# Optimization experiments

Hardware: AMD Instinct MI355X
Metric: run time of the kernel (lower is better)

## Reference

```python
import jax, jax.numpy as jnp
import numpy as np

TOP_K = 8
NORM_TOPK_PROB = False


def setup_inputs() -> dict:
    key = jax.random.key(0)
    k1, k2 = jax.random.split(key)
    hidden_states = jax.random.normal(k1, (4, 8192, 2048), dtype=jnp.float32)
    # gate weight: [n_experts=64, hidden_dim=2048], like nn.Linear weight
    weight = jax.random.normal(k2, (64, 2048), dtype=jnp.float32) * 0.02
    return {"hidden_states": hidden_states, "weight": weight}


def reference(hidden_states, weight):
    hidden_dim = weight.shape[1]
    x = hidden_states.reshape(-1, hidden_dim)            # [N, D]
    router_logits = jnp.einsum('nd,ed->ne', x, weight)   # [N, E] F.linear
    # softmax in float32 (dtype=torch.float), returned as the "logits"
    router_probs = jax.nn.softmax(router_logits.astype(jnp.float32), axis=-1)
    router_top_value, router_indices = jax.lax.top_k(router_probs, TOP_K)
    if NORM_TOPK_PROB:
        router_top_value = router_top_value / jnp.sum(router_top_value, axis=-1, keepdims=True)
    router_top_value = router_top_value.astype(router_probs.dtype)
    return (router_probs, router_top_value, router_indices)
```

## Files before the change

kernel.cpp:

```cpp
#include <hip/hip_runtime.h>
#include <math.h>


constexpr int HD = 2048, NE = 64, RPB = 64, BK = 64, NT = HD / BK, TOPK = 8;
constexpr float XSC = 4096.f;
constexpr float WSC = 8192.f;
constexpr float DESCALE = 1.0f / (XSC * WSC);

typedef _Float16 f16x8 __attribute__((ext_vector_type(8)));
typedef float f32x4 __attribute__((ext_vector_type(4)));
typedef void __attribute__((address_space(1)))* gas_t;
typedef void __attribute__((address_space(3)))* las_t;

__device__ __forceinline__ void gload_lds16(const float* g, void* l) {
  __builtin_amdgcn_global_load_lds((gas_t)(uintptr_t)g, (las_t)l, 16, 0, 0);
}

__global__ __launch_bounds__(256, 2)
void router_k(const float* __restrict__ X, const float* __restrict__ W,
              float* __restrict__ probs, float* __restrict__ topv,
              float* __restrict__ topi) {
  __shared__ float4 smem4[4096];
  char* smem = (char*)smem4;

  const int tid = threadIdx.x, wv = tid >> 6, lane = tid & 63;
  const int m_l = lane & 15, q_l = lane >> 4;
  const int rowbase = blockIdx.x * RPB;

  const int kq_st = m_l ^ ((4 * wv + q_l) & 15);
  const float* gx = X + (size_t)(rowbase + 4 * wv + q_l) * HD + kq_st * 4;

  const int we = tid >> 2, wq = tid & 3;
  const float* gw = W + (size_t)we * HD + wq * 16;
  const int g0 = we * 8 + ((2 * wq) ^ (we & 7));
  const int g1 = we * 8 + ((2 * wq + 1) ^ (we & 7));

#pragma unroll
  for (int m = 0; m < 4; ++m)
    gload_lds16(gx + (size_t)m * 16 * HD, smem + (4 * m + wv) * 1024);
  float4 wr[4];
#pragma unroll
  for (int j = 0; j < 4; ++j) wr[j] = *(const float4*)(gw + j * 4);

  f32x4 acc_hh[4], acc_cr[4];
#pragma unroll
  for (int nt = 0; nt < 4; ++nt) {
    acc_hh[nt] = {0.f, 0.f, 0.f, 0.f};
    acc_cr[nt] = {0.f, 0.f, 0.f, 0.f};
  }

  for (int t = 0; t < NT; ++t) {
    const int cur = t & 1;
    char* xcur = smem + cur * 16384;
    char* wcur = smem + 32768 + cur * 16384;

    {
      float v[16];
#pragma unroll
      for (int j = 0; j < 4; ++j) {
        v[4 * j] = wr[j].x; v[4 * j + 1] = wr[j].y;
        v[4 * j + 2] = wr[j].z; v[4 * j + 3] = wr[j].w;
      }
      f16x8 h0, h1, l0, l1;
#pragma unroll
      for (int j = 0; j < 8; ++j) {
        float a = v[j] * WSC;     _Float16 ha = (_Float16)a;
        h0[j] = ha; l0[j] = (_Float16)(a - (float)ha);
        float b = v[j + 8] * WSC; _Float16 hb = (_Float16)b;
        h1[j] = hb; l1[j] = (_Float16)(b - (float)hb);
      }
      *(f16x8*)(wcur + g0 * 16) = h0;
      *(f16x8*)(wcur + g1 * 16) = h1;
      *(f16x8*)(wcur + 8192 + g0 * 16) = l0;
      *(f16x8*)(wcur + 8192 + g1 * 16) = l1;
    }
    if (t + 1 < NT) {
#pragma unroll
      for (int j = 0; j < 4; ++j)
        wr[j] = *(const float4*)(gw + (t + 1) * BK + j * 4);
    }
    __syncthreads();
    if (t + 1 < NT) {
      char* xnxt = smem + (1 - cur) * 16384;
#pragma unroll
      for (int m = 0; m < 4; ++m)
        gload_lds16(gx + (size_t)m * 16 * HD + (t + 1) * BK, xnxt + (4 * m + wv) * 1024);
    }

#pragma unroll
    for (int s = 0; s < 2; ++s) {
      const int row_l = 16 * wv + m_l;
      const int kq0 = 8 * s + 2 * q_l;
      const int G0 = row_l * 16 + (kq0 ^ m_l);
      const int G1 = row_l * 16 + ((kq0 + 1) ^ m_l);
      f32x4 xa = *(const f32x4*)(xcur + G0 * 16);
      f32x4 xb = *(const f32x4*)(xcur + G1 * 16);
      f16x8 ah, al;
#pragma unroll
      for (int j = 0; j < 4; ++j) {
        float a = xa[j] * XSC; _Float16 ha = (_Float16)a;
        ah[j] = ha; al[j] = (_Float16)(a - (float)ha);
        float b = xb[j] * XSC; _Float16 hb = (_Float16)b;
        ah[j + 4] = hb; al[j + 4] = (_Float16)(b - (float)hb);
      }
      const int kgB = 4 * s + q_l;
#pragma unroll
      for (int nt = 0; nt < 4; ++nt) {
        const int ee = nt * 16 + m_l;
        const int gb = ee * 8 + (kgB ^ (ee & 7));
        f16x8 bh = *(const f16x8*)(wcur + gb * 16);
        f16x8 bl = *(const f16x8*)(wcur + 8192 + gb * 16);
        acc_hh[nt] = __builtin_amdgcn_mfma_f32_16x16x32_f16(ah, bh, acc_hh[nt], 0, 0, 0);
        acc_cr[nt] = __builtin_amdgcn_mfma_f32_16x16x32_f16(ah, bl, acc_cr[nt], 0, 0, 0);
        acc_cr[nt] = __builtin_amdgcn_mfma_f32_16x16x32_f16(al, bh, acc_cr[nt], 0, 0, 0);
      }
    }
  }

  __syncthreads();
  float* plds = (float*)smem;
#pragma unroll
  for (int nt = 0; nt < 4; ++nt)
#pragma unroll
    for (int r = 0; r < 4; ++r)
      plds[(16 * wv + 4 * q_l + r) * 68 + nt * 16 + m_l] =
          (acc_hh[nt][r] + acc_cr[nt][r]) * DESCALE;
  __syncthreads();

  for (int rr = 0; rr < 16; ++rr) {
    const int row_l = wv * 16 + rr;
    const float lg = plds[row_l * 68 + lane];

    float mx = lg;
#pragma unroll
    for (int off = 32; off; off >>= 1)
      mx = fmaxf(mx, __shfl_xor(mx, off, 64));

    const float ex = expf(lg - mx);
    float sm = ex;
#pragma unroll
    for (int off = 32; off; off >>= 1)
      sm += __shfl_xor(sm, off, 64);

    const float p = ex * (1.0f / sm);
    probs[(size_t)(rowbase + row_l) * NE + lane] = p;

    int rank = 0;
#pragma unroll
    for (int j = 0; j < NE; ++j) {
      const float pj = __shfl(p, j, 64);
      rank += (pj > p) || (pj == p && j < lane);
    }
    if (rank < TOPK) {
      topv[(size_t)(rowbase + row_l) * TOPK + rank] = p;
      topi[(size_t)(rowbase + row_l) * TOPK + rank] = (float)lane;
    }
  }
}

extern "C" void kernel_launch(void* const* d_in, const int* in_sizes, int n_in,
                              void* d_out, int out_size, void* d_ws, size_t ws_size,
                              hipStream_t stream) {
  const float* X = (const float*)d_in[0];
  const float* W = (const float*)d_in[1];
  const int n = in_sizes[0] / HD;

  float* probs = (float*)d_out;
  float* topv  = probs + (size_t)n * NE;
  float* topi  = topv + (size_t)n * TOPK;

  dim3 grid(n / RPB), block(256);
  hipLaunchKernelGGL(router_k, grid, block, 0, stream, X, W, probs, topv, topi);
}
```

Baseline: 423.4 us.

## Pre-split weights to fp16 hi/lo once and stream operands directly from global

Adds a small prep kernel that converts the gate weights into fp16 hi/lo pairs in workspace, so the router kernel no longer re-splits weights per block. The router now loads X and the prepared weights straight from global into registers with a three-deep software rotation, dropping the LDS staging and the per-tile barriers. Each block handles 32 rows, with two waves splitting the hidden dimension and their partial logits summed in LDS before the softmax and top-k. The trade-off is an extra launch, more global weight traffic per block (served from cache), and uncoalesced per-lane X loads.

```diff
diff --git a/kernel.cpp b/kernel.cpp
--- a/kernel.cpp
+++ b/kernel.cpp
@@ -2,45 +2,44 @@
 #include <math.h>
 
 
-constexpr int HD = 2048, NE = 64, RPB = 64, BK = 64, NT = HD / BK, TOPK = 8;
+constexpr int HD = 2048, NE = 64, TOPK = 8;
 constexpr float XSC = 4096.f;
 constexpr float WSC = 8192.f;
 constexpr float DESCALE = 1.0f / (XSC * WSC);
 
 typedef _Float16 f16x8 __attribute__((ext_vector_type(8)));
 typedef float f32x4 __attribute__((ext_vector_type(4)));
-typedef void __attribute__((address_space(1)))* gas_t;
-typedef void __attribute__((address_space(3)))* las_t;
 
-__device__ __forceinline__ void gload_lds16(const float* g, void* l) {
-  __builtin_amdgcn_global_load_lds((gas_t)(uintptr_t)g, (las_t)l, 16, 0, 0);
+__global__ __launch_bounds__(256)
+void wprep_k(const float* __restrict__ W, char* __restrict__ WP) {
+  const int n = blockIdx.x, t = threadIdx.x;
+  const float* src = W + n * HD + t * 8;
+  f16x8 hi, lo;
+#pragma unroll
+  for (int j = 0; j < 8; ++j) {
+    float a = src[j] * WSC;
+    _Float16 h = (_Float16)a;
+    hi[j] = h;
+    lo[j] = (_Float16)(a - (float)h);
+  }
+  char* dst = WP + n * 8192 + t * 32;
+  *(f16x8*)dst = hi;
+  *(f16x8*)(dst + 16) = lo;
 }
 
-__global__ __launch_bounds__(256, 2)
-void router_k(const float* __restrict__ X, const float* __restrict__ W,
+__global__ __launch_bounds__(256, 4)
+void router_k(const float* __restrict__ X, const char* __restrict__ WP,
               float* __restrict__ probs, float* __restrict__ topv,
               float* __restrict__ topi) {
-  __shared__ float4 smem4[4096];
-  char* smem = (char*)smem4;
+  __shared__ float part[4][16][68];
 
   const int tid = threadIdx.x, wv = tid >> 6, lane = tid & 63;
-  const int m_l = lane & 15, q_l = lane >> 4;
-  const int rowbase = blockIdx.x * RPB;
+  const int m = lane & 15, q = lane >> 4;
+  const int rowbase = blockIdx.x * 32;
+  const int rg = wv >> 1, h = wv & 1;
 
-  const int kq_st = m_l ^ ((4 * wv + q_l) & 15);
-  const float* gx = X + (size_t)(rowbase + 4 * wv + q_l) * HD + kq_st * 4;
-
-  const int we = tid >> 2, wq = tid & 3;
-  const float* gw = W + (size_t)we * HD + wq * 16;
-  const int g0 = we * 8 + ((2 * wq) ^ (we & 7));
-  const int g1 = we * 8 + ((2 * wq + 1) ^ (we & 7));
-
-#pragma unroll
-  for (int m = 0; m < 4; ++m)
-    gload_lds16(gx + (size_t)m * 16 * HD, smem + (4 * m + wv) * 1024);
-  float4 wr[4];
-#pragma unroll
-  for (int j = 0; j < 4; ++j) wr[j] = *(const float4*)(gw + j * 4);
+  const float* xp = X + (size_t)(rowbase + rg * 16 + m) * HD + h * 1024 + q * 8;
+  const char* wp0 = WP + m * 8192 + h * 4096 + q * 32;
 
   f32x4 acc_hh[4], acc_cr[4];
 #pragma unroll
@@ -49,87 +48,53 @@
     acc_cr[nt] = {0.f, 0.f, 0.f, 0.f};
   }
 
-  for (int t = 0; t < NT; ++t) {
-    const int cur = t & 1;
-    char* xcur = smem + cur * 16384;
-    char* wcur = smem + 32768 + cur * 16384;
+  f32x4 xaA, xbA, xaB, xbB, xaC, xbC;
+  f16x8 wf[8];
 
-    {
-      float v[16];
-#pragma unroll
-      for (int j = 0; j < 4; ++j) {
-        v[4 * j] = wr[j].x; v[4 * j + 1] = wr[j].y;
-        v[4 * j + 2] = wr[j].z; v[4 * j + 3] = wr[j].w;
-      }
-      f16x8 h0, h1, l0, l1;
-#pragma unroll
-      for (int j = 0; j < 8; ++j) {
-        float a = v[j] * WSC;     _Float16 ha = (_Float16)a;
-        h0[j] = ha; l0[j] = (_Float16)(a - (float)ha);
-        float b = v[j + 8] * WSC; _Float16 hb = (_Float16)b;
-        h1[j] = hb; l1[j] = (_Float16)(b - (float)hb);
-      }
-      *(f16x8*)(wcur + g0 * 16) = h0;
-      *(f16x8*)(wcur + g1 * 16) = h1;
-      *(f16x8*)(wcur + 8192 + g0 * 16) = l0;
-      *(f16x8*)(wcur + 8192 + g1 * 16) = l1;
-    }
-    if (t + 1 < NT) {
-#pragma unroll
-      for (int j = 0; j < 4; ++j)
-        wr[j] = *(const float4*)(gw + (t + 1) * BK + j * 4);
-    }
-    __syncthreads();
-    if (t + 1 < NT) {
-      char* xnxt = smem + (1 - cur) * 16384;
-#pragma unroll
-      for (int m = 0; m < 4; ++m)
-        gload_lds16(gx + (size_t)m * 16 * HD + (t + 1) * BK, xnxt + (4 * m + wv) * 1024);
-    }
+#define LOADX(XA, XB, kk) { XA = *(const f32x4*)(xp + (kk) * 32);          \
+                            XB = *(const f32x4*)(xp + (kk) * 32 + 4); }
+#define LOADW(kk) { _Pragma("unroll")                                      \
+    for (int nt = 0; nt < 4; ++nt) {                                       \
+      wf[2*nt]   = *(const f16x8*)(wp0 + nt * 131072 + (kk) * 128);        \
+      wf[2*nt+1] = *(const f16x8*)(wp0 + nt * 131072 + (kk) * 128 + 16); } }
+#define STEP(XA, XB) {                                                     \
+    f16x8 ah, al;                                                          \
+    _Pragma("unroll") for (int j = 0; j < 4; ++j) {                        \
+      float a = XA[j] * XSC; _Float16 ha = (_Float16)a;                    \
+      ah[j] = ha; al[j] = (_Float16)(a - (float)ha);                       \
+      float b = XB[j] * XSC; _Float16 hb = (_Float16)b;                    \
+      ah[j+4] = hb; al[j+4] = (_Float16)(b - (float)hb); }                 \
+    _Pragma("unroll") for (int nt = 0; nt < 4; ++nt) {                     \
+      acc_hh[nt] = __builtin_amdgcn_mfma_f32_16x16x32_f16(ah, wf[2*nt],   acc_hh[nt], 0, 0, 0); \
+      acc_cr[nt] = __builtin_amdgcn_mfma_f32_16x16x32_f16(ah, wf[2*nt+1], acc_cr[nt], 0, 0, 0); \
+      acc_cr[nt] = __builtin_amdgcn_mfma_f32_16x16x32_f16(al, wf[2*nt],   acc_cr[nt], 0, 0, 0); } }
 
-#pragma unroll
-    for (int s = 0; s < 2; ++s) {
-      const int row_l = 16 * wv + m_l;
-      const int kq0 = 8 * s + 2 * q_l;
-      const int G0 = row_l * 16 + (kq0 ^ m_l);
-      const int G1 = row_l * 16 + ((kq0 + 1) ^ m_l);
-      f32x4 xa = *(const f32x4*)(xcur + G0 * 16);
-      f32x4 xb = *(const f32x4*)(xcur + G1 * 16);
-      f16x8 ah, al;
-#pragma unroll
-      for (int j = 0; j < 4; ++j) {
-        float a = xa[j] * XSC; _Float16 ha = (_Float16)a;
-        ah[j] = ha; al[j] = (_Float16)(a - (float)ha);
-        float b = xb[j] * XSC; _Float16 hb = (_Float16)b;
-        ah[j + 4] = hb; al[j + 4] = (_Float16)(b - (float)hb);
-      }
-      const int kgB = 4 * s + q_l;
-#pragma unroll
-      for (int nt = 0; nt < 4; ++nt) {
-        const int ee = nt * 16 + m_l;
-        const int gb = ee * 8 + (kgB ^ (ee & 7));
-        f16x8 bh = *(const f16x8*)(wcur + gb * 16);
-        f16x8 bl = *(const f16x8*)(wcur + 8192 + gb * 16);
-        acc_hh[nt] = __builtin_amdgcn_mfma_f32_16x16x32_f16(ah, bh, acc_hh[nt], 0, 0, 0);
-        acc_cr[nt] = __builtin_amdgcn_mfma_f32_16x16x32_f16(ah, bl, acc_cr[nt], 0, 0, 0);
-        acc_cr[nt] = __builtin_amdgcn_mfma_f32_16x16x32_f16(al, bh, acc_cr[nt], 0, 0, 0);
-      }
-    }
+  LOADX(xaA, xbA, 0);
+  LOADX(xaB, xbB, 1);
+  for (int k3 = 0; k3 < 10; ++k3) {
+    const int k0 = 3 * k3;
+    LOADX(xaC, xbC, k0 + 2);  LOADW(k0);      STEP(xaA, xbA);
+    LOADX(xaA, xbA, k0 + 3);  LOADW(k0 + 1);  STEP(xaB, xbB);
+    LOADX(xaB, xbB, k0 + 4);  LOADW(k0 + 2);  STEP(xaC, xbC);
   }
+  LOADW(30);  STEP(xaA, xbA);
+  LOADW(31);  STEP(xaB, xbB);
 
-  __syncthreads();
-  float* plds = (float*)smem;
+#undef LOADX
+#undef LOADW
+#undef STEP
+
 #pragma unroll
   for (int nt = 0; nt < 4; ++nt)
 #pragma unroll
     for (int r = 0; r < 4; ++r)
-      plds[(16 * wv + 4 * q_l + r) * 68 + nt * 16 + m_l] =
-          (acc_hh[nt][r] + acc_cr[nt][r]) * DESCALE;
+      part[wv][4 * q + r][nt * 16 + m] = (acc_hh[nt][r] + acc_cr[nt][r]) * DESCALE;
   __syncthreads();
 
-  for (int rr = 0; rr < 16; ++rr) {
-    const int row_l = wv * 16 + rr;
-    const float lg = plds[row_l * 68 + lane];
+  for (int rr = 0; rr < 8; ++rr) {
+    const int rb = wv * 8 + rr;
+    const int pi = (rb >> 4) * 2, ri = rb & 15;
+    const float lg = part[pi][ri][lane] + part[pi + 1][ri][lane];
 
     float mx = lg;
 #pragma unroll
@@ -143,7 +108,7 @@
       sm += __shfl_xor(sm, off, 64);
 
     const float p = ex * (1.0f / sm);
-    probs[(size_t)(rowbase + row_l) * NE + lane] = p;
+    probs[(size_t)(rowbase + rb) * NE + lane] = p;
 
     int rank = 0;
 #pragma unroll
@@ -152,8 +117,8 @@
       rank += (pj > p) || (pj == p && j < lane);
     }
     if (rank < TOPK) {
-      topv[(size_t)(rowbase + row_l) * TOPK + rank] = p;
-      topi[(size_t)(rowbase + row_l) * TOPK + rank] = (float)lane;
+      topv[(size_t)(rowbase + rb) * TOPK + rank] = p;
+      topi[(size_t)(rowbase + rb) * TOPK + rank] = (float)lane;
     }
   }
 }
@@ -168,7 +133,9 @@
   float* probs = (float*)d_out;
   float* topv  = probs + (size_t)n * NE;
   float* topi  = topv + (size_t)n * TOPK;
+  char* WP = (char*)d_ws;
 
-  dim3 grid(n / RPB), block(256);
-  hipLaunchKernelGGL(router_k, grid, block, 0, stream, X, W, probs, topv, topi);
+  hipLaunchKernelGGL(wprep_k, dim3(NE), dim3(256), 0, stream, W, WP);
+  hipLaunchKernelGGL(router_k, dim3(n / 32), dim3(256), 0, stream,
+                     X, WP, probs, topv, topi);
 }
```

New measurement: 457.8 us. +8.1%, slower.

## Precompute split-fp16 weights in prep kernel and triple-buffer X loads

Applied to the files above, without the earlier changes.

Adds a small prep kernel that converts the gate weight into hi/lo fp16 halves once, already laid out in MFMA fragment order, and stores them in workspace. The main kernel now streams these prepared tiles straight into LDS with async global-to-LDS loads instead of converting weights per block every iteration. X gets a three-stage buffer with two tiles prefetched ahead, using explicit vmcnt waits and raw barriers. This removes redundant weight conversion and register staging from every block. In exchange it adds a second kernel launch, more LDS per block, and hand-tuned waitcnt logic that could be fragile.

```diff
diff --git a/kernel.cpp b/kernel.cpp
--- a/kernel.cpp
+++ b/kernel.cpp
@@ -12,15 +12,34 @@
 typedef void __attribute__((address_space(1)))* gas_t;
 typedef void __attribute__((address_space(3)))* las_t;
 
-__device__ __forceinline__ void gload_lds16(const float* g, void* l) {
+__device__ __forceinline__ void gload_lds16(const void* g, void* l) {
   __builtin_amdgcn_global_load_lds((gas_t)(uintptr_t)g, (las_t)l, 16, 0, 0);
 }
 
+__global__ __launch_bounds__(256)
+void wprep_k(const float* __restrict__ W, char* __restrict__ WP) {
+  const int b = blockIdx.x;
+  const int t = threadIdx.x;
+  const int nt = t >> 6, q = (t >> 4) & 3, m = t & 15;
+  const float* src = W + (size_t)(nt * 16 + m) * HD + b * 32 + q * 8;
+  f16x8 hi, lo;
+#pragma unroll
+  for (int j = 0; j < 8; ++j) {
+    float a = src[j] * WSC;
+    _Float16 ha = (_Float16)a;
+    hi[j] = ha;
+    lo[j] = (_Float16)(a - (float)ha);
+  }
+  char* dst = WP + ((size_t)b * 8 + nt * 2) * 1024 + (q * 16 + m) * 16;
+  *(f16x8*)dst = hi;
+  *(f16x8*)(dst + 1024) = lo;
+}
+
 __global__ __launch_bounds__(256, 2)
-void router_k(const float* __restrict__ X, const float* __restrict__ W,
+void router_k(const float* __restrict__ X, const char* __restrict__ WP,
               float* __restrict__ probs, float* __restrict__ topv,
               float* __restrict__ topi) {
-  __shared__ float4 smem4[4096];
+  __shared__ float4 smem4[5120];
   char* smem = (char*)smem4;
 
   const int tid = threadIdx.x, wv = tid >> 6, lane = tid & 63;
@@ -29,18 +48,7 @@
 
   const int kq_st = m_l ^ ((4 * wv + q_l) & 15);
   const float* gx = X + (size_t)(rowbase + 4 * wv + q_l) * HD + kq_st * 4;
-
-  const int we = tid >> 2, wq = tid & 3;
-  const float* gw = W + (size_t)we * HD + wq * 16;
-  const int g0 = we * 8 + ((2 * wq) ^ (we & 7));
-  const int g1 = we * 8 + ((2 * wq + 1) ^ (we & 7));
-
-#pragma unroll
-  for (int m = 0; m < 4; ++m)
-    gload_lds16(gx + (size_t)m * 16 * HD, smem + (4 * m + wv) * 1024);
-  float4 wr[4];
-#pragma unroll
-  for (int j = 0; j < 4; ++j) wr[j] = *(const float4*)(gw + j * 4);
+  const char* gw = WP + lane * 16;
 
   f32x4 acc_hh[4], acc_cr[4];
 #pragma unroll
@@ -49,44 +57,47 @@
     acc_cr[nt] = {0.f, 0.f, 0.f, 0.f};
   }
 
+#pragma unroll
+  for (int j = 0; j < 4; ++j)
+    gload_lds16(gw + (4 * wv + j) * 1024, smem + 49152 + (4 * wv + j) * 1024);
+  __builtin_amdgcn_sched_barrier(0);
+#pragma unroll
+  for (int m = 0; m < 4; ++m)
+    gload_lds16(gx + (size_t)m * 16 * HD, smem + (4 * m + wv) * 1024);
+  __builtin_amdgcn_sched_barrier(0);
+#pragma unroll
+  for (int m = 0; m < 4; ++m)
+    gload_lds16(gx + (size_t)m * 16 * HD + BK, smem + 16384 + (4 * m + wv) * 1024);
+  __builtin_amdgcn_sched_barrier(0);
+
+  int xc = 0, xn = 2;
   for (int t = 0; t < NT; ++t) {
-    const int cur = t & 1;
-    char* xcur = smem + cur * 16384;
-    char* wcur = smem + 32768 + cur * 16384;
+    if (t == NT - 1) {
+      asm volatile("s_waitcnt vmcnt(0)" ::: "memory");
+    } else {
+      asm volatile("s_waitcnt vmcnt(4)" ::: "memory");
+    }
+    __builtin_amdgcn_s_barrier();
+    __builtin_amdgcn_sched_barrier(0);
 
-    {
-      float v[16];
-#pragma unroll
-      for (int j = 0; j < 4; ++j) {
-        v[4 * j] = wr[j].x; v[4 * j + 1] = wr[j].y;
-        v[4 * j + 2] = wr[j].z; v[4 * j + 3] = wr[j].w;
-      }
-      f16x8 h0, h1, l0, l1;
-#pragma unroll
-      for (int j = 0; j < 8; ++j) {
-        float a = v[j] * WSC;     _Float16 ha = (_Float16)a;
-        h0[j] = ha; l0[j] = (_Float16)(a - (float)ha);
-        float b = v[j + 8] * WSC; _Float16 hb = (_Float16)b;
-        h1[j] = hb; l1[j] = (_Float16)(b - (float)hb);
-      }
-      *(f16x8*)(wcur + g0 * 16) = h0;
-      *(f16x8*)(wcur + g1 * 16) = h1;
-      *(f16x8*)(wcur + 8192 + g0 * 16) = l0;
-      *(f16x8*)(wcur + 8192 + g1 * 16) = l1;
-    }
     if (t + 1 < NT) {
+      char* wd = smem + 49152 + ((t + 1) & 1) * 16384;
+      const char* ws = gw + (size_t)(t + 1) * 16384;
 #pragma unroll
       for (int j = 0; j < 4; ++j)
-        wr[j] = *(const float4*)(gw + (t + 1) * BK + j * 4);
+        gload_lds16(ws + (4 * wv + j) * 1024, wd + (4 * wv + j) * 1024);
     }
-    __syncthreads();
-    if (t + 1 < NT) {
-      char* xnxt = smem + (1 - cur) * 16384;
+    __builtin_amdgcn_sched_barrier(0);
+    if (t + 2 < NT) {
+      char* xd = smem + xn * 16384;
 #pragma unroll
       for (int m = 0; m < 4; ++m)
-        gload_lds16(gx + (size_t)m * 16 * HD + (t + 1) * BK, xnxt + (4 * m + wv) * 1024);
+        gload_lds16(gx + (size_t)m * 16 * HD + (t + 2) * BK, xd + (4 * m + wv) * 1024);
     }
+    __builtin_amdgcn_sched_barrier(0);
 
+    char* xcur = smem + xc * 16384;
+    char* wcur = smem + 49152 + (t & 1) * 16384;
 #pragma unroll
     for (int s = 0; s < 2; ++s) {
       const int row_l = 16 * wv + m_l;
@@ -103,18 +114,17 @@
         float b = xb[j] * XSC; _Float16 hb = (_Float16)b;
         ah[j + 4] = hb; al[j + 4] = (_Float16)(b - (float)hb);
       }
-      const int kgB = 4 * s + q_l;
 #pragma unroll
       for (int nt = 0; nt < 4; ++nt) {
-        const int ee = nt * 16 + m_l;
-        const int gb = ee * 8 + (kgB ^ (ee & 7));
-        f16x8 bh = *(const f16x8*)(wcur + gb * 16);
-        f16x8 bl = *(const f16x8*)(wcur + 8192 + gb * 16);
+        f16x8 bh = *(const f16x8*)(wcur + (s * 8 + nt * 2) * 1024 + lane * 16);
+        f16x8 bl = *(const f16x8*)(wcur + (s * 8 + nt * 2 + 1) * 1024 + lane * 16);
         acc_hh[nt] = __builtin_amdgcn_mfma_f32_16x16x32_f16(ah, bh, acc_hh[nt], 0, 0, 0);
         acc_cr[nt] = __builtin_amdgcn_mfma_f32_16x16x32_f16(ah, bl, acc_cr[nt], 0, 0, 0);
         acc_cr[nt] = __builtin_amdgcn_mfma_f32_16x16x32_f16(al, bh, acc_cr[nt], 0, 0, 0);
       }
     }
+    xc = (xc + 1 < 3) ? xc + 1 : 0;
+    xn = (xn + 1 < 3) ? xn + 1 : 0;
   }
 
   __syncthreads();
@@ -168,7 +178,9 @@
   float* probs = (float*)d_out;
   float* topv  = probs + (size_t)n * NE;
   float* topi  = topv + (size_t)n * TOPK;
+  char* WP = (char*)d_ws;
 
-  dim3 grid(n / RPB), block(256);
-  hipLaunchKernelGGL(router_k, grid, block, 0, stream, X, W, probs, topv, topi);
+  hipLaunchKernelGGL(wprep_k, dim3(64), dim3(256), 0, stream, W, WP);
+  hipLaunchKernelGGL(router_k, dim3(n / RPB), dim3(256), 0, stream,
+                     X, WP, probs, topv, topi);
 }
```

Result: no change. 425.8 us (+0.6%).
